# Optimization experiments

Measured on AMD Instinct MI355X. Metric: run time of the kernel, lower is better.

The kernel has to match this reference:

```python
import jax, jax.numpy as jnp
import numpy as np

B = 512      # batch
T = 32       # time steps -> T-1 = 31 recurrent steps
Tm1 = T - 1
D = 256      # input_size (exogenous features)
HE = 512     # encoder hidden
HD = 512     # decoder hidden


def setup_inputs() -> dict:
    key = jax.random.key(0)
    ks = jax.random.split(key, 24)
    n = lambda k, shape, s=0.05: jax.random.normal(k, shape, dtype=jnp.float32) * s
    return dict(
        inputs=jax.random.normal(ks[0], (B, Tm1, D + 1), dtype=jnp.float32),
        enc_Wih=n(ks[1], (4 * HE, D)), enc_Whh=n(ks[2], (4 * HE, HE)),
        enc_bih=n(ks[3], (4 * HE,)), enc_bhh=n(ks[4], (4 * HE,)),
        enc_Wc=n(ks[5], (Tm1, 2 * HE)), enc_bc=n(ks[6], (Tm1,)),
        enc_Wd=n(ks[7], (Tm1, Tm1)), enc_bd=n(ks[8], (Tm1,)),
        enc_Wa=n(ks[9], (1, Tm1)), enc_ba=n(ks[10], (1,)),
        dec_W1=n(ks[11], (HE, 2 * HD + HE)), dec_b1=n(ks[12], (HE,)),
        dec_W2=n(ks[13], (1, HE)), dec_b2=n(ks[14], (1,)),
        dec_Wih=n(ks[15], (4 * HD, 1)), dec_Whh=n(ks[16], (4 * HD, HD)),
        dec_bih=n(ks[17], (4 * HD,)), dec_bhh=n(ks[18], (4 * HD,)),
        fc_W=n(ks[19], (1, HE + 1), 1.0),  # torch code does fc.weight.data.normal_() (std=1)
        fc_b=n(ks[20], (1,)),
        fcf_W=n(ks[21], (1, HD + HE)), fcf_b=n(ks[22], (1,)),
    )


def _lstm_step(x, h, c, Wih, Whh, bih, bhh):
    # single-step PyTorch LSTM; gate order i, f, g, o
    g = x @ Wih.T + bih + h @ Whh.T + bhh
    i, f, gg, o = jnp.split(g, 4, axis=-1)
    c2 = jax.nn.sigmoid(f) * c + jax.nn.sigmoid(i) * jnp.tanh(gg)
    return jax.nn.sigmoid(o) * jnp.tanh(c2), c2


def reference(inputs, enc_Wih, enc_Whh, enc_bih, enc_bhh, enc_Wc, enc_bc,
              enc_Wd, enc_bd, enc_Wa, enc_ba, dec_W1, dec_b1, dec_W2, dec_b2,
              dec_Wih, dec_Whh, dec_bih, dec_bhh, fc_W, fc_b, fcf_W, fcf_b):
    Bn = inputs.shape[0]
    y_hist = inputs[:, :, :1]   # idx_target = 0 -> [B, Tm1, 1]
    X = inputs[:, :, 1:]        # [B, Tm1, D]

    # linear_data(input_data.permute(0,2,1)) is time-invariant: [B, D, Tm1]
    t2 = jnp.einsum('btd,st->bds', X, enc_Wd) + enc_bd

    # ---- Encoder: input attention + LSTM over Tm1 steps ----
    def enc_step(carry, x_t):
        h, c = carry  # [B, HE] each
        # hidden/state are identical per input feature -> compute linear_concat once
        t1 = jnp.concatenate([h, c], axis=-1) @ enc_Wc.T + enc_bc        # [B, Tm1]
        score = jnp.tanh(t1[:, None, :] + t2) @ enc_Wa[0] + enc_ba[0]     # [B, D]
        attn = jax.nn.softmax(score, axis=1)
        w = attn * x_t                                                    # [B, D]
        h2, c2 = _lstm_step(w, h, c, enc_Wih, enc_Whh, enc_bih, enc_bhh)
        return (h2, c2), h2

    h0 = jnp.zeros((Bn, HE), dtype=inputs.dtype)
    (_, _), enc_h = jax.lax.scan(enc_step, (h0, h0), jnp.swapaxes(X, 0, 1))
    enc_out = jnp.swapaxes(enc_h, 0, 1)  # [B, Tm1, HE]

    # ---- Decoder: temporal attention + LSTM over Tm1 steps ----
    def dec_step(carry, y_t):
        h, c, _ = carry
        hs = jnp.concatenate([h, c], axis=-1)  # [B, 2*HD]
        x = jnp.concatenate(
            [jnp.broadcast_to(hs[:, None, :], (Bn, Tm1, 2 * HD)), enc_out], axis=-1)
        score = jnp.tanh(x @ dec_W1.T + dec_b1) @ dec_W2[0] + dec_b2[0]   # [B, Tm1]
        a = jax.nn.softmax(score, axis=1)
        ctx = jnp.einsum('bt,bte->be', a, enc_out)                        # [B, HE]
        y_tilde = jnp.concatenate([ctx, y_t], axis=-1) @ fc_W.T + fc_b    # [B, 1]
        h2, c2 = _lstm_step(y_tilde, h, c, dec_Wih, dec_Whh, dec_bih, dec_bhh)
        return (h2, c2, ctx), None

    hd0 = jnp.zeros((Bn, HD), dtype=inputs.dtype)
    ctx0 = jnp.zeros((Bn, HE), dtype=inputs.dtype)
    (hT, _, ctxT), _ = jax.lax.scan(dec_step, (hd0, hd0, ctx0),
                                    jnp.swapaxes(y_hist, 0, 1))
    return jnp.concatenate([hT, ctxT], axis=-1) @ fcf_W.T + fcf_b  # [B, 1]
```

## Files before the change

### kernel.cpp

```cpp
#include <hip/hip_runtime.h>
#include <math.h>

#define BATCH 512
#define TM1   31
#define DIMD  256

typedef _Float16 f16;
typedef _Float16 half8 __attribute__((ext_vector_type(8)));
typedef float floatx16 __attribute__((ext_vector_type(16)));

__device__ __forceinline__ float sigmf(float x) { return 1.f / (1.f + __expf(-x)); }

__device__ __forceinline__ float tanh_fast(float x) {
    float ax = fabsf(x);
    float t  = __expf(-2.f * ax);
    float r  = (1.f - t) / (1.f + t);
    return copysignf(r, x);
}

__device__ __forceinline__ void split16(float x, f16* hi, f16* lo) {
    f16 h = (f16)x;
    *hi = h;
    *lo = (f16)(x - (float)h);
}

__device__ __forceinline__ float blockReduceSum256(float v, float* sred) {
#pragma unroll
    for (int m = 32; m > 0; m >>= 1) v += __shfl_xor(v, m);
    __syncthreads();
    if ((threadIdx.x & 63) == 0) sred[threadIdx.x >> 6] = v;
    __syncthreads();
    return sred[0] + sred[1] + sred[2] + sred[3];
}

__device__ __forceinline__ float blockReduceMax256(float v, float* sred) {
#pragma unroll
    for (int m = 32; m > 0; m >>= 1) v = fmaxf(v, __shfl_xor(v, m));
    __syncthreads();
    if ((threadIdx.x & 63) == 0) sred[threadIdx.x >> 6] = v;
    __syncthreads();
    return fmaxf(fmaxf(sred[0], sred[1]), fmaxf(sred[2], sred[3]));
}

__global__ __launch_bounds__(256) void prep_t2s_kernel(
    const float* __restrict__ inputs,
    const float* __restrict__ eWih, const float* __restrict__ eWhh,
    const float* __restrict__ ebih, const float* __restrict__ ebhh,
    const float* __restrict__ dW1,  const float* __restrict__ dWhh,
    const float* __restrict__ dbih, const float* __restrict__ dbhh,
    const float* __restrict__ Wd,   const float* __restrict__ bd,
    f16* __restrict__ eWhi, f16* __restrict__ eWlo,
    f16* __restrict__ dWchi, f16* __restrict__ dWclo,
    f16* __restrict__ Vwhi, f16* __restrict__ Vwlo,
    float* __restrict__ ebcomb, float* __restrict__ dbias,
    float* __restrict__ t2s)
{
    __shared__ float sX[TM1 * DIMD];
    __shared__ float sWd[TM1 * TM1];
    int b = blockIdx.x, tid = threadIdx.x;
    int idx = b * 256 + tid;
    const int stride = 512 * 256;

    for (int i = tid; i < TM1 * DIMD; i += 256) {
        int tt = i >> 8, d = i & 255;
        sX[i] = inputs[((size_t)b * TM1 + tt) * 257 + 1 + d];
    }
    for (int i = tid; i < TM1 * TM1; i += 256) sWd[i] = Wd[i];
    __syncthreads();
    int d = tid;
    for (int s = 0; s < TM1; s++) {
        float acc = bd[s];
        for (int tt = 0; tt < TM1; tt++) acc += sX[tt * DIMD + d] * sWd[s * TM1 + tt];
        t2s[((size_t)b * TM1 + s) * DIMD + d] = acc;
    }

    for (int g = idx; g < 2048 * 96; g += stride) {
        int n = g / 96, k0 = (g % 96) * 8;
        const float* src = (k0 < 256) ? (eWih + n * 256 + k0)
                                      : (eWhh + n * 512 + (k0 - 256));
        float4 v0 = *(const float4*)src;
        float4 v1 = *(const float4*)(src + 4);
        float vv[8] = {v0.x, v0.y, v0.z, v0.w, v1.x, v1.y, v1.z, v1.w};
        f16 hi[8], lo[8];
#pragma unroll
        for (int e = 0; e < 8; e++) split16(vv[e], &hi[e], &lo[e]);
        *(half8*)(eWhi + n * 768 + k0) = *(half8*)hi;
        *(half8*)(eWlo + n * 768 + k0) = *(half8*)lo;
    }
    for (int g = idx; g < 2560 * 128; g += stride) {
        int n = g >> 7, k0 = (g & 127) * 8;
        float vv[8] = {};
        if (n < 512) {
            const float* src = dW1 + n * 1536 + k0;
            float4 v0 = *(const float4*)src, v1 = *(const float4*)(src + 4);
            vv[0]=v0.x; vv[1]=v0.y; vv[2]=v0.z; vv[3]=v0.w;
            vv[4]=v1.x; vv[5]=v1.y; vv[6]=v1.z; vv[7]=v1.w;
        } else if (k0 < 512) {
            const float* src = dWhh + (n - 512) * 512 + k0;
            float4 v0 = *(const float4*)src, v1 = *(const float4*)(src + 4);
            vv[0]=v0.x; vv[1]=v0.y; vv[2]=v0.z; vv[3]=v0.w;
            vv[4]=v1.x; vv[5]=v1.y; vv[6]=v1.z; vv[7]=v1.w;
        }
        f16 hi[8], lo[8];
#pragma unroll
        for (int e = 0; e < 8; e++) split16(vv[e], &hi[e], &lo[e]);
        *(half8*)(dWchi + n * 1024 + k0) = *(half8*)hi;
        *(half8*)(dWclo + n * 1024 + k0) = *(half8*)lo;
    }
    for (int g = idx; g < 512 * 64; g += stride) {
        int n = g >> 6, k0 = (g & 63) * 8;
        const float* src = dW1 + n * 1536 + 1024 + k0;
        float4 v0 = *(const float4*)src, v1 = *(const float4*)(src + 4);
        float vv[8] = {v0.x, v0.y, v0.z, v0.w, v1.x, v1.y, v1.z, v1.w};
        f16 hi[8], lo[8];
#pragma unroll
        for (int e = 0; e < 8; e++) split16(vv[e], &hi[e], &lo[e]);
        *(half8*)(Vwhi + n * 512 + k0) = *(half8*)hi;
        *(half8*)(Vwlo + n * 512 + k0) = *(half8*)lo;
    }
    for (int i = idx; i < 2048; i += stride) ebcomb[i] = ebih[i] + ebhh[i];
    for (int i = idx; i < 2560; i += stride)
        dbias[i] = (i < 512) ? 0.f : (dbih[i - 512] + dbhh[i - 512]);
}

__global__ __launch_bounds__(256) void gemm2f(
    const f16* __restrict__ Ahi, int lda,
    const f16* __restrict__ Whi, const f16* __restrict__ Wlo, int ldw,
    const float* __restrict__ bias, f16* __restrict__ C, int ldc,
    long long Cstride, int K, int nsplit, int NT, int MT, int KS, int NREP)
{
    __shared__ f16 sAh[64 * 64];
    __shared__ f16 sWh[64 * 64];
    __shared__ f16 sWl[64 * 64];
    int tid = threadIdx.x, bid = blockIdx.x;
    int nbase = bid % NT;
    int m0 = ((bid / NT) % MT) * 64;
    int ks = bid / (NT * MT);
    int lane = tid & 63, wid = tid >> 6;
    int wm = wid >> 1, wn = wid & 1;
    int rl = lane & 31, kq = lane >> 5;

    int sr = tid >> 2;
    int g0 = (tid & 3) * 2;
    int s0 = sr * 64 + ((g0 ^ (sr & 7)) * 8);
    int s1 = sr * 64 + (((g0 + 1) ^ (sr & 7)) * 8);
    int arow = (wm * 32 + rl) * 64;
    int wrow = (wn * 32 + rl) * 64;
    int sw = (rl & 7);

    const f16* pAh = Ahi + (size_t)(m0 + sr) * lda + g0 * 8;
    f16* Cp = C + (size_t)ks * Cstride;

    for (int r = 0; r < NREP; ++r) {
        int n0 = (nbase + r * NT) * 64;
        int Kfull = (n0 >= nsplit) ? 512 : K;
        int ksz = Kfull / KS;
        int kbeg = ks * ksz, kend = kbeg + ksz;
        const f16* pWh = Whi + (size_t)(n0 + sr) * ldw + g0 * 8;
        const f16* pWl = Wlo + (size_t)(n0 + sr) * ldw + g0 * 8;

        float4 rAh0 = *(const float4*)(pAh + kbeg);
        float4 rAh1 = *(const float4*)(pAh + kbeg + 8);
        float4 rWh0 = *(const float4*)(pWh + kbeg);
        float4 rWh1 = *(const float4*)(pWh + kbeg + 8);
        float4 rWl0 = *(const float4*)(pWl + kbeg);
        float4 rWl1 = *(const float4*)(pWl + kbeg + 8);

        floatx16 acc = {};

        for (int k0 = kbeg; k0 < kend; k0 += 64) {
            __syncthreads();
            *(float4*)&sAh[s0] = rAh0; *(float4*)&sAh[s1] = rAh1;
            *(float4*)&sWh[s0] = rWh0; *(float4*)&sWh[s1] = rWh1;
            *(float4*)&sWl[s0] = rWl0; *(float4*)&sWl[s1] = rWl1;
            __syncthreads();
            int kn = k0 + 64;
            if (kn < kend) {
                rAh0 = *(const float4*)(pAh + kn); rAh1 = *(const float4*)(pAh + kn + 8);
                rWh0 = *(const float4*)(pWh + kn); rWh1 = *(const float4*)(pWh + kn + 8);
                rWl0 = *(const float4*)(pWl + kn); rWl1 = *(const float4*)(pWl + kn + 8);
            }
#pragma unroll
            for (int kk = 0; kk < 64; kk += 16) {
                int lg = (kk >> 3) + kq;
                int off = ((lg ^ sw) * 8);
                half8 ah = *(const half8*)&sAh[arow + off];
                half8 wh = *(const half8*)&sWh[wrow + off];
                half8 wl = *(const half8*)&sWl[wrow + off];
                acc = __builtin_amdgcn_mfma_f32_32x32x16_f16(ah, wh, acc, 0, 0, 0);
                acc = __builtin_amdgcn_mfma_f32_32x32x16_f16(ah, wl, acc, 0, 0, 0);
            }
        }

        int col = n0 + wn * 32 + rl;
        float bv = (ks == 0) ? bias[col] : 0.f;
#pragma unroll
        for (int rr = 0; rr < 16; ++rr) {
            int row = m0 + wm * 32 + (rr & 3) + 8 * (rr >> 2) + 4 * kq;
            Cp[(size_t)row * ldc + col] = (f16)(acc[rr] + bv);
        }
    }
}

__global__ __launch_bounds__(256) void enc_step_kernel(
    const float* __restrict__ inputs, const float* __restrict__ t2s,
    const float* __restrict__ Wc, const float* __restrict__ bc,
    const float* __restrict__ Wa, const float* __restrict__ ba,
    const f16* __restrict__ g, long long gstride,
    float* __restrict__ hc,
    f16* __restrict__ Ahi, f16* __restrict__ enchi,
    float* __restrict__ hc_dec, f16* __restrict__ hdhi,
    int t) {
    __shared__ float sh_hc[1024];
    __shared__ float t1s[32];
    __shared__ float sred[4];
    int b = blockIdx.x, tid = threadIdx.x;

    if (t > 0) {
        for (int e = tid; e < 512; e += 256) {
            const f16* gp = g + (size_t)b * 2048 + e;
            float gi = (float)gp[0]    + (float)gp[gstride];
            float gf = (float)gp[512]  + (float)gp[gstride + 512];
            float gg = (float)gp[1024] + (float)gp[gstride + 1024];
            float go = (float)gp[1536] + (float)gp[gstride + 1536];
            float cp = hc[b * 1024 + 512 + e];
            float c2 = sigmf(gf) * cp + sigmf(gi) * tanh_fast(gg);
            float h2 = sigmf(go) * tanh_fast(c2);
            hc[b * 1024 + e] = h2;
            hc[b * 1024 + 512 + e] = c2;
            sh_hc[e] = h2;
            sh_hc[512 + e] = c2;
            enchi[((size_t)b * TM1 + (t - 1)) * 512 + e] = (f16)h2;
        }
    } else {
        for (int j = tid; j < 1024; j += 256) { sh_hc[j] = 0.f; hc[b * 1024 + j] = 0.f; }
    }
    if (t == TM1) {
        for (int j = tid; j < 1024; j += 256) {
            hc_dec[b * 1024 + j] = 0.f;
            hdhi[b * 1024 + j] = (f16)0.f;
        }
        return;
    }
    __syncthreads();

    if (tid < 248) {
        int s = tid >> 3, l8 = tid & 7;
        const float* wrow = Wc + s * 1024;
        float p = 0.f;
        for (int j = l8 * 4; j < 1024; j += 32) {
            float4 w4 = *(const float4*)(wrow + j);
            float4 h4 = *(const float4*)(&sh_hc[j]);
            p += w4.x * h4.x + w4.y * h4.y + w4.z * h4.z + w4.w * h4.w;
        }
        p += __shfl_xor(p, 1); p += __shfl_xor(p, 2); p += __shfl_xor(p, 4);
        if (l8 == 0) t1s[s] = p + bc[s];
    }
    __syncthreads();

    int d = tid;
    float sc = ba[0];
    const float* t2p = t2s + ((size_t)b * TM1) * DIMD + d;
    for (int s = 0; s < TM1; s++) sc += tanh_fast(t1s[s] + t2p[s * DIMD]) * Wa[s];
    float mx = blockReduceMax256(sc, sred);
    float ex = __expf(sc - mx);
    float sm = blockReduceSum256(ex, sred);
    float w = (ex / sm) * inputs[((size_t)b * TM1 + t) * 257 + 1 + d];
    Ahi[b * 768 + d] = (f16)w;
    for (int j = tid; j < 512; j += 256)
        Ahi[b * 768 + 256 + j] = (f16)sh_hc[j];
}

__global__ __launch_bounds__(256) void dec_step_kernel(
    const float* __restrict__ inputs, const f16* __restrict__ V,
    const float* __restrict__ W2, const float* __restrict__ b2,
    const f16* __restrict__ enchi,
    const float* __restrict__ fcW, const float* __restrict__ fcb,
    const float* __restrict__ Wih,
    const f16* __restrict__ gu, long long ustride,
    float* __restrict__ hc, f16* __restrict__ hdhi,
    const float* __restrict__ fcfW, const float* __restrict__ fcfb,
    float* __restrict__ out, int t) {
    __shared__ float su[512];
    __shared__ float sw2[512];
    __shared__ float s_att[TM1];
    __shared__ float sred[4];
    int b = blockIdx.x, tid = threadIdx.x;
    const bool last = (t == TM1 - 1);
    for (int e = tid; e < 512; e += 256) {
        const f16* q = gu + (size_t)b * 2560 + e;
        su[e]  = (float)q[0] + (float)q[ustride];
        sw2[e] = W2[e];
    }
    __syncthreads();
    if (tid < 248) {
        int tp = tid >> 3, l8 = tid & 7;
        const f16* vrow = V + ((size_t)b * TM1 + tp) * 512;
        float p = 0.f;
        for (int j = l8 * 8; j < 512; j += 64) {
            half8 v8 = *(const half8*)(vrow + j);
#pragma unroll
            for (int e = 0; e < 8; e++)
                p += tanh_fast(su[j + e] + (float)v8[e]) * sw2[j + e];
        }
        p += __shfl_xor(p, 1); p += __shfl_xor(p, 2); p += __shfl_xor(p, 4);
        if (l8 == 0) s_att[tp] = p + b2[0];
    }
    __syncthreads();
    if (tid < 64) {
        float v = (tid < TM1) ? s_att[tid] : -3.4e38f;
        float m = v;
#pragma unroll
        for (int k = 32; k > 0; k >>= 1) m = fmaxf(m, __shfl_xor(m, k));
        float e = (tid < TM1) ? __expf(v - m) : 0.f;
        float s = e;
#pragma unroll
        for (int k = 32; k > 0; k >>= 1) s += __shfl_xor(s, k);
        if (tid < TM1) s_att[tid] = e / s;
    }
    __syncthreads();

    float part = 0.f;
    float pctx = 0.f;
#pragma unroll
    for (int r = 0; r < 2; r++) {
        int e = tid + r * 256;
        float cx = 0.f;
        const f16* eh = enchi + (size_t)b * TM1 * 512 + e;
        for (int tp = 0; tp < TM1; tp++)
            cx += s_att[tp] * (float)eh[tp * 512];
        part += cx * fcW[e];
        if (last) pctx += cx * fcfW[512 + e];
    }
    float y = inputs[((size_t)b * TM1 + t) * 257];
    float ysum = blockReduceSum256(part, sred);
    float y_til = ysum + y * fcW[512] + fcb[0];

    float ph = 0.f;
    for (int e = tid; e < 512; e += 256) {
        const f16* q = gu + (size_t)b * 2560 + e;
        float gi = (float)q[512]  + (float)q[ustride + 512]  + y_til * Wih[e];
        float gf = (float)q[1024] + (float)q[ustride + 1024] + y_til * Wih[512 + e];
        float gg = (float)q[1536] + (float)q[ustride + 1536] + y_til * Wih[1024 + e];
        float go = (float)q[2048] + (float)q[ustride + 2048] + y_til * Wih[1536 + e];
        float cp = hc[b * 1024 + 512 + e];
        float c2 = sigmf(gf) * cp + sigmf(gi) * tanh_fast(gg);
        float h2 = sigmf(go) * tanh_fast(c2);
        if (!last) {
            hc[b * 1024 + e] = h2;
            hc[b * 1024 + 512 + e] = c2;
            hdhi[(size_t)b * 1024 + e] = (f16)h2;
            hdhi[(size_t)b * 1024 + 512 + e] = (f16)c2;
        } else {
            ph += h2 * fcfW[e];
        }
    }
    if (last) {
        float s = blockReduceSum256(ph + pctx, sred);
        if (tid == 0) out[b] = s + fcfb[0];
    }
}

extern "C" void kernel_launch(void* const* d_in, const int* in_sizes, int n_in,
                              void* d_out, int out_size, void* d_ws, size_t ws_size,
                              hipStream_t stream) {
    const float* inputs  = (const float*)d_in[0];
    const float* eWih    = (const float*)d_in[1];
    const float* eWhh    = (const float*)d_in[2];
    const float* ebih    = (const float*)d_in[3];
    const float* ebhh    = (const float*)d_in[4];
    const float* eWc     = (const float*)d_in[5];
    const float* ebc     = (const float*)d_in[6];
    const float* eWd     = (const float*)d_in[7];
    const float* ebd     = (const float*)d_in[8];
    const float* eWa     = (const float*)d_in[9];
    const float* eba     = (const float*)d_in[10];
    const float* dW1     = (const float*)d_in[11];
    const float* db1     = (const float*)d_in[12];
    const float* dW2     = (const float*)d_in[13];
    const float* db2     = (const float*)d_in[14];
    const float* dWih    = (const float*)d_in[15];
    const float* dWhh    = (const float*)d_in[16];
    const float* dbih    = (const float*)d_in[17];
    const float* dbhh    = (const float*)d_in[18];
    const float* fcW     = (const float*)d_in[19];
    const float* fcb     = (const float*)d_in[20];
    const float* fcfW    = (const float*)d_in[21];
    const float* fcfb    = (const float*)d_in[22];
    float* out = (float*)d_out;

    float* scr = (float*)d_ws;
    float* t2s = scr;
    f16*   Vf  = (f16*)scr;
    f16* g0e = (f16*)(scr + 4063232);
    f16* gu0 = (f16*)(scr + 4063232);
    float* hc_enc = scr + 5373952;
    f16*   Ahi    = (f16*)(scr + 5898240);
    float* hc_dec = scr + 6094848;
    f16*   hdhi   = (f16*)(scr + 6619136);
    f16* fp = (f16*)(scr + 6881280);
    f16* eWhi  = fp;             fp += 1572864;
    f16* eWlo  = fp;             fp += 1572864;
    f16* dWchi = fp;             fp += 2621440;
    f16* dWclo = fp;             fp += 2621440;
    f16* Vwhi  = fp;             fp += 262144;
    f16* Vwlo  = fp;             fp += 262144;
    f16* enchi = fp;             fp += 8126464;
    float* ebcomb = (float*)(((uintptr_t)fp + 15) & ~(uintptr_t)15);
    float* dbias  = ebcomb + 2048;

    hipLaunchKernelGGL(prep_t2s_kernel, dim3(512), dim3(256), 0, stream,
                       inputs, eWih, eWhh, ebih, ebhh, dW1, dWhh, dbih, dbhh,
                       eWd, ebd, eWhi, eWlo, dWchi, dWclo, Vwhi, Vwlo,
                       ebcomb, dbias, t2s);

    const long long gstride = 1048576;
    const long long ustride = 1310720;

    for (int t = 0; t < TM1; t++) {
        hipLaunchKernelGGL(enc_step_kernel, dim3(BATCH), dim3(256), 0, stream,
                           inputs, t2s, eWc, ebc, eWa, eba, g0e, gstride, hc_enc,
                           Ahi, enchi, hc_dec, hdhi, t);
        hipLaunchKernelGGL(gemm2f, dim3(512), dim3(256), 0, stream,
                           Ahi, 768, eWhi, eWlo, 768, ebcomb,
                           g0e, 2048, gstride, 768, 1 << 30, 32, 8, 2, 1);
    }
    hipLaunchKernelGGL(enc_step_kernel, dim3(BATCH), dim3(256), 0, stream,
                       inputs, t2s, eWc, ebc, eWa, eba, g0e, gstride, hc_enc,
                       Ahi, enchi, hc_dec, hdhi, TM1);

    hipLaunchKernelGGL(gemm2f, dim3(992), dim3(256), 0, stream,
                       enchi, 512, Vwhi, Vwlo, 512, db1,
                       Vf, 512, 0, 512, 1 << 30, 4, 248, 1, 2);

    for (int t = 0; t < TM1; t++) {
        hipLaunchKernelGGL(gemm2f, dim3(640), dim3(256), 0, stream,
                           hdhi, 1024, dWchi, dWclo, 1024, dbias,
                           gu0, 2560, ustride, 1024, 512, 40, 8, 2, 1);
        hipLaunchKernelGGL(dec_step_kernel, dim3(BATCH), dim3(256), 0, stream,
                           inputs, Vf, dW2, db2, enchi, fcW, fcb, dWih,
                           gu0, ustride, hc_dec, hdhi, fcfW, fcfb, out, t);
    }
}
```

Before: 1.769 ms.

## Raise split-K to four slices in step GEMMs, store t2s in fp16

The per-step encoder and decoder GEMMs now use four K-slices instead of two, doubling the grid size so the GPU has more blocks to run. The LSTM pointwise stages sum four partial outputs and are vectorised to process two elements per thread. The time-invariant attention term t2s is stored in fp16 to cut the memory read each encoder step. The cost is more partial-sum traffic, a relaid scratch buffer, and lower precision in the attention scores.

```diff
diff --git a/kernel.cpp b/kernel.cpp
--- a/kernel.cpp
+++ b/kernel.cpp
@@ -6,6 +6,7 @@
 #define DIMD  256
 
 typedef _Float16 f16;
+typedef _Float16 half2v __attribute__((ext_vector_type(2)));
 typedef _Float16 half8 __attribute__((ext_vector_type(8)));
 typedef float floatx16 __attribute__((ext_vector_type(16)));
 
@@ -53,7 +54,7 @@
     f16* __restrict__ dWchi, f16* __restrict__ dWclo,
     f16* __restrict__ Vwhi, f16* __restrict__ Vwlo,
     float* __restrict__ ebcomb, float* __restrict__ dbias,
-    float* __restrict__ t2s)
+    f16* __restrict__ t2s)
 {
     __shared__ float sX[TM1 * DIMD];
     __shared__ float sWd[TM1 * TM1];
@@ -71,7 +72,7 @@
     for (int s = 0; s < TM1; s++) {
         float acc = bd[s];
         for (int tt = 0; tt < TM1; tt++) acc += sX[tt * DIMD + d] * sWd[s * TM1 + tt];
-        t2s[((size_t)b * TM1 + s) * DIMD + d] = acc;
+        t2s[((size_t)b * TM1 + s) * DIMD + d] = (f16)acc;
     }
 
     for (int g = idx; g < 2048 * 96; g += stride) {
@@ -203,7 +204,7 @@
 }
 
 __global__ __launch_bounds__(256) void enc_step_kernel(
-    const float* __restrict__ inputs, const float* __restrict__ t2s,
+    const float* __restrict__ inputs, const f16* __restrict__ t2s,
     const float* __restrict__ Wc, const float* __restrict__ bc,
     const float* __restrict__ Wa, const float* __restrict__ ba,
     const f16* __restrict__ g, long long gstride,
@@ -217,21 +218,33 @@
     int b = blockIdx.x, tid = threadIdx.x;
 
     if (t > 0) {
-        for (int e = tid; e < 512; e += 256) {
-            const f16* gp = g + (size_t)b * 2048 + e;
-            float gi = (float)gp[0]    + (float)gp[gstride];
-            float gf = (float)gp[512]  + (float)gp[gstride + 512];
-            float gg = (float)gp[1024] + (float)gp[gstride + 1024];
-            float go = (float)gp[1536] + (float)gp[gstride + 1536];
-            float cp = hc[b * 1024 + 512 + e];
-            float c2 = sigmf(gf) * cp + sigmf(gi) * tanh_fast(gg);
-            float h2 = sigmf(go) * tanh_fast(c2);
-            hc[b * 1024 + e] = h2;
-            hc[b * 1024 + 512 + e] = c2;
-            sh_hc[e] = h2;
-            sh_hc[512 + e] = c2;
-            enchi[((size_t)b * TM1 + (t - 1)) * 512 + e] = (f16)h2;
-        }
+        int e = tid * 2;
+        const f16* gp = g + (size_t)b * 2048 + e;
+        float gi0 = 0.f, gi1 = 0.f, gf0 = 0.f, gf1 = 0.f;
+        float gg0 = 0.f, gg1 = 0.f, go0 = 0.f, go1 = 0.f;
+#pragma unroll
+        for (int s = 0; s < 4; s++) {
+            const f16* q = gp + s * gstride;
+            half2v a = *(const half2v*)(q);
+            half2v f = *(const half2v*)(q + 512);
+            half2v gv = *(const half2v*)(q + 1024);
+            half2v o = *(const half2v*)(q + 1536);
+            gi0 += (float)a[0]; gi1 += (float)a[1];
+            gf0 += (float)f[0]; gf1 += (float)f[1];
+            gg0 += (float)gv[0]; gg1 += (float)gv[1];
+            go0 += (float)o[0]; go1 += (float)o[1];
+        }
+        float2 cpv = *(const float2*)(hc + b * 1024 + 512 + e);
+        float c20 = sigmf(gf0) * cpv.x + sigmf(gi0) * tanh_fast(gg0);
+        float c21 = sigmf(gf1) * cpv.y + sigmf(gi1) * tanh_fast(gg1);
+        float h20 = sigmf(go0) * tanh_fast(c20);
+        float h21 = sigmf(go1) * tanh_fast(c21);
+        *(float2*)(hc + b * 1024 + e) = make_float2(h20, h21);
+        *(float2*)(hc + b * 1024 + 512 + e) = make_float2(c20, c21);
+        sh_hc[e] = h20; sh_hc[e + 1] = h21;
+        sh_hc[512 + e] = c20; sh_hc[512 + e + 1] = c21;
+        half2v hv; hv[0] = (f16)h20; hv[1] = (f16)h21;
+        *(half2v*)(enchi + ((size_t)b * TM1 + (t - 1)) * 512 + e) = hv;
     } else {
         for (int j = tid; j < 1024; j += 256) { sh_hc[j] = 0.f; hc[b * 1024 + j] = 0.f; }
     }
@@ -260,8 +273,8 @@
 
     int d = tid;
     float sc = ba[0];
-    const float* t2p = t2s + ((size_t)b * TM1) * DIMD + d;
-    for (int s = 0; s < TM1; s++) sc += tanh_fast(t1s[s] + t2p[s * DIMD]) * Wa[s];
+    const f16* t2p = t2s + ((size_t)b * TM1) * DIMD + d;
+    for (int s = 0; s < TM1; s++) sc += tanh_fast(t1s[s] + (float)t2p[s * DIMD]) * Wa[s];
     float mx = blockReduceMax256(sc, sred);
     float ex = __expf(sc - mx);
     float sm = blockReduceSum256(ex, sred);
@@ -287,10 +300,17 @@
     __shared__ float sred[4];
     int b = blockIdx.x, tid = threadIdx.x;
     const bool last = (t == TM1 - 1);
-    for (int e = tid; e < 512; e += 256) {
+    {
+        int e = tid * 2;
         const f16* q = gu + (size_t)b * 2560 + e;
-        su[e]  = (float)q[0] + (float)q[ustride];
-        sw2[e] = W2[e];
+        float u0 = 0.f, u1 = 0.f;
+#pragma unroll
+        for (int s = 0; s < 4; s++) {
+            half2v a = *(const half2v*)(q + s * ustride);
+            u0 += (float)a[0]; u1 += (float)a[1];
+        }
+        su[e] = u0; su[e + 1] = u1;
+        sw2[e] = W2[e]; sw2[e + 1] = W2[e + 1];
     }
     __syncthreads();
     if (tid < 248) {
@@ -337,22 +357,41 @@
     float y_til = ysum + y * fcW[512] + fcb[0];
 
     float ph = 0.f;
-    for (int e = tid; e < 512; e += 256) {
+    {
+        int e = tid * 2;
         const f16* q = gu + (size_t)b * 2560 + e;
-        float gi = (float)q[512]  + (float)q[ustride + 512]  + y_til * Wih[e];
-        float gf = (float)q[1024] + (float)q[ustride + 1024] + y_til * Wih[512 + e];
-        float gg = (float)q[1536] + (float)q[ustride + 1536] + y_til * Wih[1024 + e];
-        float go = (float)q[2048] + (float)q[ustride + 2048] + y_til * Wih[1536 + e];
-        float cp = hc[b * 1024 + 512 + e];
-        float c2 = sigmf(gf) * cp + sigmf(gi) * tanh_fast(gg);
-        float h2 = sigmf(go) * tanh_fast(c2);
+        float gi0 = 0.f, gi1 = 0.f, gf0 = 0.f, gf1 = 0.f;
+        float gg0 = 0.f, gg1 = 0.f, go0 = 0.f, go1 = 0.f;
+#pragma unroll
+        for (int s = 0; s < 4; s++) {
+            const f16* qq = q + s * ustride;
+            half2v a = *(const half2v*)(qq + 512);
+            half2v f = *(const half2v*)(qq + 1024);
+            half2v gv = *(const half2v*)(qq + 1536);
+            half2v o = *(const half2v*)(qq + 2048);
+            gi0 += (float)a[0]; gi1 += (float)a[1];
+            gf0 += (float)f[0]; gf1 += (float)f[1];
+            gg0 += (float)gv[0]; gg1 += (float)gv[1];
+            go0 += (float)o[0]; go1 += (float)o[1];
+        }
+        gi0 += y_til * Wih[e];        gi1 += y_til * Wih[e + 1];
+        gf0 += y_til * Wih[512 + e];  gf1 += y_til * Wih[512 + e + 1];
+        gg0 += y_til * Wih[1024 + e]; gg1 += y_til * Wih[1024 + e + 1];
+        go0 += y_til * Wih[1536 + e]; go1 += y_til * Wih[1536 + e + 1];
+        float2 cpv = *(const float2*)(hc + b * 1024 + 512 + e);
+        float c20 = sigmf(gf0) * cpv.x + sigmf(gi0) * tanh_fast(gg0);
+        float c21 = sigmf(gf1) * cpv.y + sigmf(gi1) * tanh_fast(gg1);
+        float h20 = sigmf(go0) * tanh_fast(c20);
+        float h21 = sigmf(go1) * tanh_fast(c21);
         if (!last) {
-            hc[b * 1024 + e] = h2;
-            hc[b * 1024 + 512 + e] = c2;
-            hdhi[(size_t)b * 1024 + e] = (f16)h2;
-            hdhi[(size_t)b * 1024 + 512 + e] = (f16)c2;
+            *(float2*)(hc + b * 1024 + e) = make_float2(h20, h21);
+            *(float2*)(hc + b * 1024 + 512 + e) = make_float2(c20, c21);
+            half2v hv; hv[0] = (f16)h20; hv[1] = (f16)h21;
+            half2v cv; cv[0] = (f16)c20; cv[1] = (f16)c21;
+            *(half2v*)(hdhi + (size_t)b * 1024 + e) = hv;
+            *(half2v*)(hdhi + (size_t)b * 1024 + 512 + e) = cv;
         } else {
-            ph += h2 * fcfW[e];
+            ph += h20 * fcfW[e] + h21 * fcfW[e + 1];
         }
     }
     if (last) {
@@ -390,15 +429,15 @@
     float* out = (float*)d_out;
 
     float* scr = (float*)d_ws;
-    float* t2s = scr;
-    f16*   Vf  = (f16*)scr;
+    f16* t2s = (f16*)scr;
+    f16* Vf  = (f16*)scr;
     f16* g0e = (f16*)(scr + 4063232);
     f16* gu0 = (f16*)(scr + 4063232);
-    float* hc_enc = scr + 5373952;
-    f16*   Ahi    = (f16*)(scr + 5898240);
-    float* hc_dec = scr + 6094848;
-    f16*   hdhi   = (f16*)(scr + 6619136);
-    f16* fp = (f16*)(scr + 6881280);
+    float* hc_enc = scr + 6684672;
+    f16*   Ahi    = (f16*)(scr + 7208960);
+    float* hc_dec = scr + 7405568;
+    f16*   hdhi   = (f16*)(scr + 7929856);
+    f16* fp = (f16*)(scr + 8192000);
     f16* eWhi  = fp;             fp += 1572864;
     f16* eWlo  = fp;             fp += 1572864;
     f16* dWchi = fp;             fp += 2621440;
@@ -421,9 +460,9 @@
         hipLaunchKernelGGL(enc_step_kernel, dim3(BATCH), dim3(256), 0, stream,
                            inputs, t2s, eWc, ebc, eWa, eba, g0e, gstride, hc_enc,
                            Ahi, enchi, hc_dec, hdhi, t);
-        hipLaunchKernelGGL(gemm2f, dim3(512), dim3(256), 0, stream,
+        hipLaunchKernelGGL(gemm2f, dim3(1024), dim3(256), 0, stream,
                            Ahi, 768, eWhi, eWlo, 768, ebcomb,
-                           g0e, 2048, gstride, 768, 1 << 30, 32, 8, 2, 1);
+                           g0e, 2048, gstride, 768, 1 << 30, 32, 8, 4, 1);
     }
     hipLaunchKernelGGL(enc_step_kernel, dim3(BATCH), dim3(256), 0, stream,
                        inputs, t2s, eWc, ebc, eWa, eba, g0e, gstride, hc_enc,
@@ -434,9 +473,9 @@
                        Vf, 512, 0, 512, 1 << 30, 4, 248, 1, 2);
 
     for (int t = 0; t < TM1; t++) {
-        hipLaunchKernelGGL(gemm2f, dim3(640), dim3(256), 0, stream,
+        hipLaunchKernelGGL(gemm2f, dim3(1280), dim3(256), 0, stream,
                            hdhi, 1024, dWchi, dWclo, 1024, dbias,
-                           gu0, 2560, ustride, 1024, 512, 40, 8, 2, 1);
+                           gu0, 2560, ustride, 1024, 512, 40, 8, 4, 1);
         hipLaunchKernelGGL(dec_step_kernel, dim3(BATCH), dim3(256), 0, stream,
                            inputs, Vf, dW2, db2, enchi, fcW, fcb, dWih,
                            gu0, ustride, hc_dec, hdhi, fcfW, fcfb, out, t);
```

Measured after the change: 1.820 ms. 1.03x slower.
